# Kernel optimization log

Hardware: AMD Instinct MI355X
Metric: run time of the kernel (lower is better)

## Reference

```python
import jax, jax.numpy as jnp
import numpy as np

IN_DIM = 2048
ATT_NUM = 40
BATCH = 4096
HID = IN_DIM // 2

def setup_inputs() -> dict:
    key = jax.random.key(0)
    k_x, k_w1, k_b1, k_w2, k_b2 = jax.random.split(key, 5)
    # per-head params stacked: head h has Linear(in_dim, hid) then Linear(hid, 1)
    s1 = 1.0 / np.sqrt(IN_DIM)
    s2 = 1.0 / np.sqrt(HID)
    return {
        "x": jax.random.normal(k_x, (BATCH, IN_DIM), dtype=jnp.float32),
        "W1": jax.random.uniform(k_w1, (ATT_NUM, IN_DIM, HID), dtype=jnp.float32, minval=-s1, maxval=s1),
        "b1": jax.random.uniform(k_b1, (ATT_NUM, HID), dtype=jnp.float32, minval=-s1, maxval=s1),
        "W2": jax.random.uniform(k_w2, (ATT_NUM, HID), dtype=jnp.float32, minval=-s2, maxval=s2),
        "b2": jax.random.uniform(k_b2, (ATT_NUM,), dtype=jnp.float32, minval=-s2, maxval=s2),
    }

def reference(x, W1, b1, W2, b2):
    # batched over heads: h[b,a,:] = gelu(x[b] @ W1[a] + b1[a])
    h = jax.nn.gelu(jnp.einsum('bd,adh->bah', x, W1) + b1, approximate=False)
    # y[b,a] = sigmoid(h[b,a] . W2[a] + b2[a])  -> matches stack/squeeze/permute to [B, att_num]
    y = jax.nn.sigmoid(jnp.einsum('bah,ah->ba', h, W2) + b2)
    return y
```

## Files before the change

kernel.cpp:

```cpp
#include <hip/hip_runtime.h>
#include <hip/hip_bf16.h>

#define IN_DIM 2048
#define HID    1024
#define ATT    40
#define BATCH  4096

#define BM 128
#define BN 128
#define BK 64

typedef unsigned short u16;
typedef __attribute__((ext_vector_type(8))) __bf16 bf16x8;
typedef __attribute__((ext_vector_type(4))) float  f32x4;

struct alignas(8)  u16x4 { u16 a, b, c, d; };
struct alignas(16) u16x8 { u16x4 lo, hi; };

__device__ __forceinline__ u16 f2bf(float f) {
    unsigned int u = __float_as_uint(f);
    unsigned int r = (u + 0x7fffu + ((u >> 16) & 1u)) >> 16;
    return (u16)r;
}
__device__ __forceinline__ float f4get(const float4& v, int j) {
    return reinterpret_cast<const float*>(&v)[j];
}

__device__ __forceinline__ void load16_to_lds(const void* g, void* l) {
    __builtin_amdgcn_global_load_lds(
        (const __attribute__((address_space(1))) unsigned int*)(uintptr_t)g,
        (__attribute__((address_space(3))) unsigned int*)(uintptr_t)l,
        16, 0, 0);
}

__global__ void convert_x(const float* __restrict__ x, u16* __restrict__ xb) {
    int i = (blockIdx.x * 256 + threadIdx.x) * 4;
    float4 v = *(const float4*)(x + i);
    u16x4 o = { f2bf(v.x), f2bf(v.y), f2bf(v.z), f2bf(v.w) };
    *(u16x4*)(xb + i) = o;
}

__global__ void transpose_w1(const float* __restrict__ W1, u16* __restrict__ W1t) {
    __shared__ u16 tile[64 * 64];
    const int a  = blockIdx.z;
    const int d0 = blockIdx.y * 64;
    const int h0 = blockIdx.x * 64;
    const float* src = W1 + (size_t)a * IN_DIM * HID + (size_t)d0 * HID + h0;
    u16* dst = W1t + (size_t)a * HID * IN_DIM + (size_t)h0 * IN_DIM + d0;

    const int tr = threadIdx.x >> 4;
    const int tc = threadIdx.x & 15;
    float4 v[4];
    #pragma unroll
    for (int p = 0; p < 4; ++p)
        v[p] = *(const float4*)(src + (size_t)(tr * 4 + p) * HID + tc * 4);
    #pragma unroll
    for (int j = 0; j < 4; ++j) {
        int h = tc * 4 + j;
        int phys = tr ^ (h & 15);
        u16x4 o = { f2bf(f4get(v[0], j)), f2bf(f4get(v[1], j)),
                    f2bf(f4get(v[2], j)), f2bf(f4get(v[3], j)) };
        *(u16x4*)&tile[h * 64 + phys * 4] = o;
    }
    __syncthreads();
    const int h8 = threadIdx.x >> 3;
    const int dc = threadIdx.x & 7;
    #pragma unroll
    for (int p = 0; p < 2; ++p) {
        int h = p * 32 + h8;
        int p0 = (2 * dc)     ^ (h & 15);
        int p1 = (2 * dc + 1) ^ (h & 15);
        u16x8 o;
        o.lo = *(const u16x4*)&tile[h * 64 + p0 * 4];
        o.hi = *(const u16x4*)&tile[h * 64 + p1 * 4];
        *(u16x8*)(dst + (size_t)h * IN_DIM + dc * 8) = o;
    }
}

__global__ __launch_bounds__(256, 3) void gemm_fused(
    const u16* __restrict__ xb,
    const u16* __restrict__ w1t,
    const float* __restrict__ b1,
    const float* __restrict__ w2,
    float* __restrict__ partial)
{
    __shared__ __align__(16) u16 smem[2 * BM * BK];
    const int a  = blockIdx.z;
    const int m0 = blockIdx.x * BM;
    const int n0 = blockIdx.y * BN;

    const int tid  = threadIdx.x;
    const int w    = tid >> 6;
    const int l    = tid & 63;
    const int quad = l >> 4;
    const int lr   = l & 15;
    const int wm   = (w >> 1) * 64;
    const int wn   = (w & 1) * 64;

    int offG[4];
    #pragma unroll
    for (int j = 0; j < 4; ++j) {
        int p   = j * 256 + tid;
        int row = p >> 3;
        int kc  = (p & 7) ^ (row & 7);
        offG[j] = row * IN_DIM + kc * 8;
    }
    int offLA[2][4], offLB[2][4];
    #pragma unroll
    for (int ks = 0; ks < 2; ++ks)
        #pragma unroll
        for (int f = 0; f < 4; ++f) {
            int rowA = wm + f * 16 + lr;
            int kcA  = (ks * 4 + quad) ^ (rowA & 7);
            offLA[ks][f] = rowA * BK + kcA * 8;
            int rowB = wn + f * 16 + lr;
            int kcB  = (ks * 4 + quad) ^ (rowB & 7);
            offLB[ks][f] = BM * BK + rowB * BK + kcB * 8;
        }

    const u16* Abase = xb + (size_t)m0 * IN_DIM;
    const u16* Bbase = w1t + (size_t)a * ((size_t)HID * IN_DIM) + (size_t)n0 * IN_DIM;

    f32x4 acc[4][4];
    #pragma unroll
    for (int i = 0; i < 4; ++i)
        #pragma unroll
        for (int j = 0; j < 4; ++j)
            acc[i][j] = (f32x4){0.f, 0.f, 0.f, 0.f};

    for (int k0 = 0; k0 < IN_DIM; k0 += BK) {
        const u16* Ak = Abase + k0;
        const u16* Bk = Bbase + k0;
        #pragma unroll
        for (int j = 0; j < 4; ++j)
            load16_to_lds(Ak + offG[j], &smem[(j * 256 + w * 64) * 8]);
        #pragma unroll
        for (int j = 0; j < 4; ++j)
            load16_to_lds(Bk + offG[j], &smem[BM * BK + (j * 256 + w * 64) * 8]);
        __syncthreads();

        #pragma unroll
        for (int ks = 0; ks < 2; ++ks) {
            bf16x8 af[4], bfr[4];
            #pragma unroll
            for (int f = 0; f < 4; ++f) af[f]  = *(const bf16x8*)&smem[offLA[ks][f]];
            #pragma unroll
            for (int f = 0; f < 4; ++f) bfr[f] = *(const bf16x8*)&smem[offLB[ks][f]];
            #pragma unroll
            for (int fm = 0; fm < 4; ++fm)
                #pragma unroll
                for (int fn = 0; fn < 4; ++fn)
                    acc[fm][fn] = __builtin_amdgcn_mfma_f32_16x16x32_bf16(
                        af[fm], bfr[fn], acc[fm][fn], 0, 0, 0);
        }
        __syncthreads();
    }

    float b1v[4], w2v[4];
    #pragma unroll
    for (int fn = 0; fn < 4; ++fn) {
        int col = n0 + wn + fn * 16 + lr;
        b1v[fn] = b1[a * HID + col];
        w2v[fn] = w2[a * HID + col];
    }
    #pragma unroll
    for (int fm = 0; fm < 4; ++fm) {
        #pragma unroll
        for (int r = 0; r < 4; ++r) {
            float s = 0.f;
            #pragma unroll
            for (int fn = 0; fn < 4; ++fn) {
                float z = acc[fm][fn][r] + b1v[fn];
                float g = 0.5f * z * (1.0f + erff(z * 0.70710678118654752f));
                s += g * w2v[fn];
            }
            s += __shfl_xor(s, 1, 64);
            s += __shfl_xor(s, 2, 64);
            s += __shfl_xor(s, 4, 64);
            s += __shfl_xor(s, 8, 64);
            if (lr == 0) {
                int grow = m0 + wm + fm * 16 + quad * 4 + r;
                atomicAdd(&partial[grow * ATT + a], s);
            }
        }
    }
}

__global__ void finish_kernel(const float* __restrict__ partial,
                              const float* __restrict__ b2,
                              float* __restrict__ out, int n) {
    int i = blockIdx.x * 256 + threadIdx.x;
    if (i < n) {
        float z = partial[i] + b2[i % ATT];
        out[i] = 1.0f / (1.0f + expf(-z));
    }
}

extern "C" void kernel_launch(void* const* d_in, const int* in_sizes, int n_in,
                              void* d_out, int out_size, void* d_ws, size_t ws_size,
                              hipStream_t stream) {
    const float* x  = (const float*)d_in[0];
    const float* W1 = (const float*)d_in[1];
    const float* b1 = (const float*)d_in[2];
    const float* W2 = (const float*)d_in[3];
    const float* b2 = (const float*)d_in[4];
    float* out = (float*)d_out;

    char* ws = (char*)d_ws;
    float* partial = (float*)ws;
    u16*   xb      = (u16*)(ws + 655360);
    u16*   w1t     = (u16*)(ws + 655360 + 16777216);

    hipMemsetAsync(partial, 0, (size_t)BATCH * ATT * sizeof(float), stream);
    convert_x<<<dim3(BATCH * IN_DIM / (256 * 4)), dim3(256), 0, stream>>>(x, xb);
    transpose_w1<<<dim3(HID / 64, IN_DIM / 64, ATT), dim3(256), 0, stream>>>(W1, w1t);
    gemm_fused<<<dim3(BATCH / BM, HID / BN, ATT), dim3(256), 0, stream>>>(
        xb, w1t, b1, W2, partial);
    finish_kernel<<<dim3((BATCH * ATT + 255) / 256), dim3(256), 0, stream>>>(
        partial, b2, out, BATCH * ATT);
}
```

Before: 1.163 ms.

## Rewrite GEMM as 256x256 tiles with 8 waves and pipelined LDS staging

The GEMM moves from 128x128 tiles with 4 waves to 256x256 tiles with 8 waves. It uses a 4-slot LDS ring where A and B half-tiles are prefetched one to two K-steps ahead, with explicit vmcnt waits, raw barriers and MFMA priority bumps so loads overlap compute. Blocks are remapped so consecutive workgroups spread across XCDs. The W1 transpose switches to 128x128 tiles with a padded LDS layout. This aims to cut global traffic per FLOP and hide memory latency, in exchange for complex hand synchronisation, more registers and a fixed grid mapping.

```diff
diff --git a/kernel.cpp b/kernel.cpp
--- a/kernel.cpp
+++ b/kernel.cpp
@@ -6,9 +6,10 @@
 #define ATT    40
 #define BATCH  4096
 
-#define BM 128
-#define BN 128
-#define BK 64
+#define GBM 256
+#define GBN 256
+#define GBK 64
+#define NT  (IN_DIM / GBK)
 
 typedef unsigned short u16;
 typedef __attribute__((ext_vector_type(8))) __bf16 bf16x8;
@@ -16,6 +17,9 @@
 
 struct alignas(8)  u16x4 { u16 a, b, c, d; };
 struct alignas(16) u16x8 { u16x4 lo, hi; };
+
+#define FENCE() asm volatile("" ::: "memory")
+#define BAR()   do { FENCE(); __builtin_amdgcn_s_barrier(); FENCE(); } while (0)
 
 __device__ __forceinline__ u16 f2bf(float f) {
     unsigned int u = __float_as_uint(f);
@@ -40,120 +44,193 @@
     *(u16x4*)(xb + i) = o;
 }
 
-__global__ void transpose_w1(const float* __restrict__ W1, u16* __restrict__ W1t) {
-    __shared__ u16 tile[64 * 64];
+__global__ __launch_bounds__(256) void transpose_w1(const float* __restrict__ W1,
+                                                    u16* __restrict__ W1t) {
+    __shared__ __align__(16) u16 tile[128 * 136];
     const int a  = blockIdx.z;
-    const int d0 = blockIdx.y * 64;
-    const int h0 = blockIdx.x * 64;
+    const int d0 = blockIdx.y * 128;
+    const int h0 = blockIdx.x * 128;
     const float* src = W1 + (size_t)a * IN_DIM * HID + (size_t)d0 * HID + h0;
     u16* dst = W1t + (size_t)a * HID * IN_DIM + (size_t)h0 * IN_DIM + d0;
 
-    const int tr = threadIdx.x >> 4;
-    const int tc = threadIdx.x & 15;
-    float4 v[4];
-    #pragma unroll
-    for (int p = 0; p < 4; ++p)
-        v[p] = *(const float4*)(src + (size_t)(tr * 4 + p) * HID + tc * 4);
-    #pragma unroll
-    for (int j = 0; j < 4; ++j) {
-        int h = tc * 4 + j;
-        int phys = tr ^ (h & 15);
-        u16x4 o = { f2bf(f4get(v[0], j)), f2bf(f4get(v[1], j)),
-                    f2bf(f4get(v[2], j)), f2bf(f4get(v[3], j)) };
-        *(u16x4*)&tile[h * 64 + phys * 4] = o;
+    const int rg = threadIdx.x >> 5;
+    const int cg = threadIdx.x & 31;
+
+    float4 v[4][4];
+    #pragma unroll
+    for (int pp = 0; pp < 4; ++pp) {
+        int r0 = pp * 32 + rg * 4;
+        #pragma unroll
+        for (int q = 0; q < 4; ++q)
+            v[pp][q] = *(const float4*)(src + (size_t)(r0 + q) * HID + cg * 4);
+    }
+    #pragma unroll
+    for (int pp = 0; pp < 4; ++pp) {
+        int r0 = pp * 32 + rg * 4;
+        #pragma unroll
+        for (int j = 0; j < 4; ++j) {
+            int h = cg * 4 + j;
+            u16x4 o = { f2bf(f4get(v[pp][0], j)), f2bf(f4get(v[pp][1], j)),
+                        f2bf(f4get(v[pp][2], j)), f2bf(f4get(v[pp][3], j)) };
+            *(u16x4*)&tile[h * 136 + r0] = o;
+        }
     }
     __syncthreads();
-    const int h8 = threadIdx.x >> 3;
-    const int dc = threadIdx.x & 7;
-    #pragma unroll
-    for (int p = 0; p < 2; ++p) {
-        int h = p * 32 + h8;
-        int p0 = (2 * dc)     ^ (h & 15);
-        int p1 = (2 * dc + 1) ^ (h & 15);
-        u16x8 o;
-        o.lo = *(const u16x4*)&tile[h * 64 + p0 * 4];
-        o.hi = *(const u16x4*)&tile[h * 64 + p1 * 4];
+    const int hg = threadIdx.x >> 4;
+    const int dc = threadIdx.x & 15;
+    #pragma unroll
+    for (int qq = 0; qq < 8; ++qq) {
+        int h = qq * 16 + hg;
+        u16x8 o = *(const u16x8*)&tile[h * 136 + dc * 8];
         *(u16x8*)(dst + (size_t)h * IN_DIM + dc * 8) = o;
     }
 }
 
-__global__ __launch_bounds__(256, 3) void gemm_fused(
+__global__ __launch_bounds__(512, 2) void gemm_fused(
     const u16* __restrict__ xb,
     const u16* __restrict__ w1t,
     const float* __restrict__ b1,
     const float* __restrict__ w2,
     float* __restrict__ partial)
 {
-    __shared__ __align__(16) u16 smem[2 * BM * BK];
-    const int a  = blockIdx.z;
-    const int m0 = blockIdx.x * BM;
-    const int n0 = blockIdx.y * BN;
-
-    const int tid  = threadIdx.x;
-    const int w    = tid >> 6;
-    const int l    = tid & 63;
-    const int quad = l >> 4;
-    const int lr   = l & 15;
-    const int wm   = (w >> 1) * 64;
-    const int wn   = (w & 1) * 64;
-
-    int offG[4];
-    #pragma unroll
-    for (int j = 0; j < 4; ++j) {
-        int p   = j * 256 + tid;
+    __shared__ __align__(16) u16 smem[65536];
+
+    const int fid = blockIdx.x + 16 * (blockIdx.y + 4 * blockIdx.z);
+    const int nf  = (fid & 7) * (2560 >> 3) + (fid >> 3);
+    const int a   = nf >> 6;
+    const int rr  = nf & 63;
+    const int m0  = (rr & 15) * GBM;
+    const int n0  = (rr >> 4) * GBN;
+
+    const int tid   = threadIdx.x;
+    const int w     = tid >> 6;
+    const int l     = tid & 63;
+    const int quad  = l >> 4;
+    const int lr    = l & 15;
+    const int mh    = w >> 2;
+    const int nh    = (w >> 1) & 1;
+    const int wm    = mh * 128;
+    const int wn    = (w & 3) * 64;
+    const int nrow0 = (w & 1) * 64;
+
+    int offS[2];
+    #pragma unroll
+    for (int j = 0; j < 2; ++j) {
+        int p   = j * 512 + tid;
         int row = p >> 3;
         int kc  = (p & 7) ^ (row & 7);
-        offG[j] = row * IN_DIM + kc * 8;
-    }
-    int offLA[2][4], offLB[2][4];
-    #pragma unroll
-    for (int ks = 0; ks < 2; ++ks)
-        #pragma unroll
-        for (int f = 0; f < 4; ++f) {
-            int rowA = wm + f * 16 + lr;
-            int kcA  = (ks * 4 + quad) ^ (rowA & 7);
-            offLA[ks][f] = rowA * BK + kcA * 8;
-            int rowB = wn + f * 16 + lr;
-            int kcB  = (ks * 4 + quad) ^ (rowB & 7);
-            offLB[ks][f] = BM * BK + rowB * BK + kcB * 8;
-        }
-
-    const u16* Abase = xb + (size_t)m0 * IN_DIM;
-    const u16* Bbase = w1t + (size_t)a * ((size_t)HID * IN_DIM) + (size_t)n0 * IN_DIM;
-
-    f32x4 acc[4][4];
-    #pragma unroll
-    for (int i = 0; i < 4; ++i)
+        offS[j] = row * IN_DIM + kc * 8;
+    }
+    const u16* Ab = xb + (size_t)m0 * IN_DIM;
+    const u16* Bb = w1t + (size_t)a * ((size_t)HID * IN_DIM) + (size_t)n0 * IN_DIM;
+
+    auto stageA = [&](int t, int h) {
+        const u16* g = Ab + (size_t)h * 128 * IN_DIM + t * GBK;
+        int sb = (((2 * t + h) & 3) << 13) + (w << 9);
+        load16_to_lds(g + offS[0], &smem[sb]);
+        load16_to_lds(g + offS[1], &smem[sb + 4096]);
+    };
+    auto stageB = [&](int t, int h) {
+        const u16* g = Bb + (size_t)h * 128 * IN_DIM + t * GBK;
+        int sb = 32768 + (((2 * t + h) & 3) << 13) + (w << 9);
+        load16_to_lds(g + offS[0], &smem[sb]);
+        load16_to_lds(g + offS[1], &smem[sb + 4096]);
+    };
+
+    f32x4 acc[8][4];
+    #pragma unroll
+    for (int i = 0; i < 8; ++i)
         #pragma unroll
         for (int j = 0; j < 4; ++j)
             acc[i][j] = (f32x4){0.f, 0.f, 0.f, 0.f};
 
-    for (int k0 = 0; k0 < IN_DIM; k0 += BK) {
-        const u16* Ak = Abase + k0;
-        const u16* Bk = Bbase + k0;
-        #pragma unroll
-        for (int j = 0; j < 4; ++j)
-            load16_to_lds(Ak + offG[j], &smem[(j * 256 + w * 64) * 8]);
-        #pragma unroll
-        for (int j = 0; j < 4; ++j)
-            load16_to_lds(Bk + offG[j], &smem[BM * BK + (j * 256 + w * 64) * 8]);
-        __syncthreads();
-
-        #pragma unroll
-        for (int ks = 0; ks < 2; ++ks) {
-            bf16x8 af[4], bfr[4];
-            #pragma unroll
-            for (int f = 0; f < 4; ++f) af[f]  = *(const bf16x8*)&smem[offLA[ks][f]];
-            #pragma unroll
-            for (int f = 0; f < 4; ++f) bfr[f] = *(const bf16x8*)&smem[offLB[ks][f]];
-            #pragma unroll
-            for (int fm = 0; fm < 4; ++fm)
-                #pragma unroll
-                for (int fn = 0; fn < 4; ++fn)
-                    acc[fm][fn] = __builtin_amdgcn_mfma_f32_16x16x32_bf16(
-                        af[fm], bfr[fn], acc[fm][fn], 0, 0, 0);
-        }
-        __syncthreads();
+    stageB(0, 0); stageB(0, 1); stageA(0, 0); stageA(0, 1); stageB(1, 0); stageB(1, 1);
+    asm volatile("s_waitcnt vmcnt(4)" ::: "memory");
+    BAR();
+
+    for (int t = 0; t < NT; ++t) {
+        const int abase = (((2 * t + mh) & 3) << 13);
+        const int bbase = 32768 + (((2 * t + nh) & 3) << 13);
+        bf16x8 af[4], bf[4];
+
+        #pragma unroll
+        for (int f = 0; f < 4; ++f) {
+            int rb = nrow0 + f * 16 + lr;
+            bf[f] = *(const bf16x8*)&smem[bbase + rb * 64 + (quad ^ (rb & 7)) * 8];
+        }
+        #pragma unroll
+        for (int f = 0; f < 4; ++f) {
+            int ra = f * 16 + lr;
+            af[f] = *(const bf16x8*)&smem[abase + ra * 64 + (quad ^ (ra & 7)) * 8];
+        }
+        if (t + 1 < NT) stageA(t + 1, 0);
+        BAR();
+        __builtin_amdgcn_s_setprio(1);
+        #pragma unroll
+        for (int fm = 0; fm < 4; ++fm)
+            #pragma unroll
+            for (int fn = 0; fn < 4; ++fn)
+                acc[fm][fn] = __builtin_amdgcn_mfma_f32_16x16x32_bf16(
+                    af[fm], bf[fn], acc[fm][fn], 0, 0, 0);
+        __builtin_amdgcn_s_setprio(0);
+        BAR();
+
+        #pragma unroll
+        for (int f = 0; f < 4; ++f) {
+            int ra = 64 + f * 16 + lr;
+            af[f] = *(const bf16x8*)&smem[abase + ra * 64 + (quad ^ (ra & 7)) * 8];
+        }
+        if (t + 1 < NT) stageA(t + 1, 1);
+        BAR();
+        __builtin_amdgcn_s_setprio(1);
+        #pragma unroll
+        for (int fm = 0; fm < 4; ++fm)
+            #pragma unroll
+            for (int fn = 0; fn < 4; ++fn)
+                acc[4 + fm][fn] = __builtin_amdgcn_mfma_f32_16x16x32_bf16(
+                    af[fm], bf[fn], acc[4 + fm][fn], 0, 0, 0);
+        __builtin_amdgcn_s_setprio(0);
+        BAR();
+
+        #pragma unroll
+        for (int f = 0; f < 4; ++f) {
+            int rb = nrow0 + f * 16 + lr;
+            bf[f] = *(const bf16x8*)&smem[bbase + rb * 64 + ((4 + quad) ^ (rb & 7)) * 8];
+        }
+        #pragma unroll
+        for (int f = 0; f < 4; ++f) {
+            int ra = f * 16 + lr;
+            af[f] = *(const bf16x8*)&smem[abase + ra * 64 + ((4 + quad) ^ (ra & 7)) * 8];
+        }
+        BAR();
+        __builtin_amdgcn_s_setprio(1);
+        #pragma unroll
+        for (int fm = 0; fm < 4; ++fm)
+            #pragma unroll
+            for (int fn = 0; fn < 4; ++fn)
+                acc[fm][fn] = __builtin_amdgcn_mfma_f32_16x16x32_bf16(
+                    af[fm], bf[fn], acc[fm][fn], 0, 0, 0);
+        __builtin_amdgcn_s_setprio(0);
+        BAR();
+
+        #pragma unroll
+        for (int f = 0; f < 4; ++f) {
+            int ra = 64 + f * 16 + lr;
+            af[f] = *(const bf16x8*)&smem[abase + ra * 64 + ((4 + quad) ^ (ra & 7)) * 8];
+        }
+        if (t + 2 < NT) { stageB(t + 2, 0); stageB(t + 2, 1); }
+        BAR();
+        __builtin_amdgcn_s_setprio(1);
+        #pragma unroll
+        for (int fm = 0; fm < 4; ++fm)
+            #pragma unroll
+            for (int fn = 0; fn < 4; ++fn)
+                acc[4 + fm][fn] = __builtin_amdgcn_mfma_f32_16x16x32_bf16(
+                    af[fm], bf[fn], acc[4 + fm][fn], 0, 0, 0);
+        __builtin_amdgcn_s_setprio(0);
+        if (t < NT - 2)       { asm volatile("s_waitcnt vmcnt(4)" ::: "memory"); }
+        else if (t == NT - 2) { asm volatile("s_waitcnt vmcnt(0)" ::: "memory"); }
+        BAR();
     }
 
     float b1v[4], w2v[4];
@@ -164,7 +241,7 @@
         w2v[fn] = w2[a * HID + col];
     }
     #pragma unroll
-    for (int fm = 0; fm < 4; ++fm) {
+    for (int fm = 0; fm < 8; ++fm) {
         #pragma unroll
         for (int r = 0; r < 4; ++r) {
             float s = 0.f;
@@ -213,8 +290,8 @@
 
     hipMemsetAsync(partial, 0, (size_t)BATCH * ATT * sizeof(float), stream);
     convert_x<<<dim3(BATCH * IN_DIM / (256 * 4)), dim3(256), 0, stream>>>(x, xb);
-    transpose_w1<<<dim3(HID / 64, IN_DIM / 64, ATT), dim3(256), 0, stream>>>(W1, w1t);
-    gemm_fused<<<dim3(BATCH / BM, HID / BN, ATT), dim3(256), 0, stream>>>(
+    transpose_w1<<<dim3(HID / 128, IN_DIM / 128, ATT), dim3(256), 0, stream>>>(W1, w1t);
+    gemm_fused<<<dim3(BATCH / GBM, HID / GBN, ATT), dim3(512), 0, stream>>>(
         xb, w1t, b1, W2, partial);
     finish_kernel<<<dim3((BATCH * ATT + 255) / 256), dim3(256), 0, stream>>>(
         partial, b2, out, BATCH * ATT);
```

New measurement: 1.177 ms. No clear change (+1.2%).

## Fuse W1 fp32-to-bf16 transpose into GEMM B-tile loading

Applied to the files above, without the earlier changes.

Removes the separate W1 transpose/convert kernel and its workspace round trip; the GEMM now loads fp32 W1 rows directly, converts to bf16 with hardware conversion, and writes transposed into swizzled LDS. This eliminates one full pass over W1 plus the bf16 write, but each GEMM block now reads twice as many bytes for B, re-reading fp32 weights for every M tile, and uses synchronous register loads instead of direct-to-LDS loads. A new XOR swizzle is applied to the B tile layout to limit bank conflicts on the transposed stores.

```diff
diff --git a/kernel.cpp b/kernel.cpp
--- a/kernel.cpp
+++ b/kernel.cpp
@@ -21,6 +21,10 @@
     unsigned int u = __float_as_uint(f);
     unsigned int r = (u + 0x7fffu + ((u >> 16) & 1u)) >> 16;
     return (u16)r;
+}
+__device__ __forceinline__ u16 f2bf_hw(float f) {
+    __bf16 h = (__bf16)f;
+    return __builtin_bit_cast(u16, h);
 }
 __device__ __forceinline__ float f4get(const float4& v, int j) {
     return reinterpret_cast<const float*>(&v)[j];
@@ -40,46 +44,9 @@
     *(u16x4*)(xb + i) = o;
 }
 
-__global__ void transpose_w1(const float* __restrict__ W1, u16* __restrict__ W1t) {
-    __shared__ u16 tile[64 * 64];
-    const int a  = blockIdx.z;
-    const int d0 = blockIdx.y * 64;
-    const int h0 = blockIdx.x * 64;
-    const float* src = W1 + (size_t)a * IN_DIM * HID + (size_t)d0 * HID + h0;
-    u16* dst = W1t + (size_t)a * HID * IN_DIM + (size_t)h0 * IN_DIM + d0;
-
-    const int tr = threadIdx.x >> 4;
-    const int tc = threadIdx.x & 15;
-    float4 v[4];
-    #pragma unroll
-    for (int p = 0; p < 4; ++p)
-        v[p] = *(const float4*)(src + (size_t)(tr * 4 + p) * HID + tc * 4);
-    #pragma unroll
-    for (int j = 0; j < 4; ++j) {
-        int h = tc * 4 + j;
-        int phys = tr ^ (h & 15);
-        u16x4 o = { f2bf(f4get(v[0], j)), f2bf(f4get(v[1], j)),
-                    f2bf(f4get(v[2], j)), f2bf(f4get(v[3], j)) };
-        *(u16x4*)&tile[h * 64 + phys * 4] = o;
-    }
-    __syncthreads();
-    const int h8 = threadIdx.x >> 3;
-    const int dc = threadIdx.x & 7;
-    #pragma unroll
-    for (int p = 0; p < 2; ++p) {
-        int h = p * 32 + h8;
-        int p0 = (2 * dc)     ^ (h & 15);
-        int p1 = (2 * dc + 1) ^ (h & 15);
-        u16x8 o;
-        o.lo = *(const u16x4*)&tile[h * 64 + p0 * 4];
-        o.hi = *(const u16x4*)&tile[h * 64 + p1 * 4];
-        *(u16x8*)(dst + (size_t)h * IN_DIM + dc * 8) = o;
-    }
-}
-
 __global__ __launch_bounds__(256, 3) void gemm_fused(
-    const u16* __restrict__ xb,
-    const u16* __restrict__ w1t,
+    const u16*  __restrict__ xb,
+    const float* __restrict__ W1,
     const float* __restrict__ b1,
     const float* __restrict__ w2,
     float* __restrict__ partial)
@@ -105,6 +72,15 @@
         int kc  = (p & 7) ^ (row & 7);
         offG[j] = row * IN_DIM + kc * 8;
     }
+    const int nn = tid & 31;
+    const int kq = tid >> 5;
+    int offWB[4];
+    #pragma unroll
+    for (int j = 0; j < 4; ++j) {
+        int n  = 4 * nn + j;
+        int sn = (n & 7) ^ ((n >> 3) & 7);
+        offWB[j] = BM * BK + n * BK + ((kq ^ sn)) * 8;
+    }
     int offLA[2][4], offLB[2][4];
     #pragma unroll
     for (int ks = 0; ks < 2; ++ks)
@@ -114,12 +90,13 @@
             int kcA  = (ks * 4 + quad) ^ (rowA & 7);
             offLA[ks][f] = rowA * BK + kcA * 8;
             int rowB = wn + f * 16 + lr;
-            int kcB  = (ks * 4 + quad) ^ (rowB & 7);
+            int sB   = (rowB & 7) ^ ((rowB >> 3) & 7);
+            int kcB  = (ks * 4 + quad) ^ sB;
             offLB[ks][f] = BM * BK + rowB * BK + kcB * 8;
         }
 
-    const u16* Abase = xb + (size_t)m0 * IN_DIM;
-    const u16* Bbase = w1t + (size_t)a * ((size_t)HID * IN_DIM) + (size_t)n0 * IN_DIM;
+    const u16*   Abase = xb + (size_t)m0 * IN_DIM;
+    const float* Bbase = W1 + (size_t)a * ((size_t)IN_DIM * HID) + n0;
 
     f32x4 acc[4][4];
     #pragma unroll
@@ -130,13 +107,23 @@
 
     for (int k0 = 0; k0 < IN_DIM; k0 += BK) {
         const u16* Ak = Abase + k0;
-        const u16* Bk = Bbase + k0;
         #pragma unroll
         for (int j = 0; j < 4; ++j)
             load16_to_lds(Ak + offG[j], &smem[(j * 256 + w * 64) * 8]);
-        #pragma unroll
-        for (int j = 0; j < 4; ++j)
-            load16_to_lds(Bk + offG[j], &smem[BM * BK + (j * 256 + w * 64) * 8]);
+        const float* Bk = Bbase + (size_t)(k0 + 8 * kq) * HID + 4 * nn;
+        #pragma unroll
+        for (int h = 0; h < 2; ++h) {
+            float4 v0 = *(const float4*)(Bk + (4 * h + 0) * HID);
+            float4 v1 = *(const float4*)(Bk + (4 * h + 1) * HID);
+            float4 v2 = *(const float4*)(Bk + (4 * h + 2) * HID);
+            float4 v3 = *(const float4*)(Bk + (4 * h + 3) * HID);
+            #pragma unroll
+            for (int j = 0; j < 4; ++j) {
+                u16x4 o = { f2bf_hw(f4get(v0, j)), f2bf_hw(f4get(v1, j)),
+                            f2bf_hw(f4get(v2, j)), f2bf_hw(f4get(v3, j)) };
+                *(u16x4*)&smem[offWB[j] + h * 4] = o;
+            }
+        }
         __syncthreads();
 
         #pragma unroll
@@ -209,13 +196,11 @@
     char* ws = (char*)d_ws;
     float* partial = (float*)ws;
     u16*   xb      = (u16*)(ws + 655360);
-    u16*   w1t     = (u16*)(ws + 655360 + 16777216);
 
     hipMemsetAsync(partial, 0, (size_t)BATCH * ATT * sizeof(float), stream);
     convert_x<<<dim3(BATCH * IN_DIM / (256 * 4)), dim3(256), 0, stream>>>(x, xb);
-    transpose_w1<<<dim3(HID / 64, IN_DIM / 64, ATT), dim3(256), 0, stream>>>(W1, w1t);
     gemm_fused<<<dim3(BATCH / BM, HID / BN, ATT), dim3(256), 0, stream>>>(
-        xb, w1t, b1, W2, partial);
+        xb, W1, b1, W2, partial);
     finish_kernel<<<dim3((BATCH * ATT + 255) / 256), dim3(256), 0, stream>>>(
         partial, b2, out, BATCH * ATT);
 }
```

New measurement: 1.356 ms. +16.6%, slower.
